# Kernel tuning notes

Hardware: AMD Instinct MI355X
Metric: run time of the kernel (lower is better)

Reference implementation:

```python
import jax, jax.numpy as jnp
import numpy as np

N = 8192
E = 262144
D_IN = 512
H1 = 32
H2 = 16
EPS = 1e-32


def setup_inputs() -> dict:
    key = jax.random.key(0)
    ks = jax.random.split(key, 7)
    X = jax.random.normal(ks[0], (N, D_IN), dtype=jnp.float32)
    edge_row = jax.random.randint(ks[1], (E,), 0, N, dtype=jnp.int64 if jax.config.read('jax_enable_x64') else jnp.int32).astype(jnp.int32)
    edge_col = jax.random.randint(ks[2], (E,), 0, N, dtype=jnp.int32)
    edge_val = jax.random.uniform(ks[3], (E,), dtype=jnp.float32)
    # glorot-style init scale (uniform in [-r, r])
    def glorot(k, din, dout):
        r = np.sqrt(6.0 / (din + dout)).astype(np.float32)
        return jax.random.uniform(k, (din, dout), dtype=jnp.float32, minval=-r, maxval=r)
    W0 = glorot(ks[4], D_IN, H1)
    W1 = glorot(ks[5], H1, H2)
    W2 = glorot(ks[6], H1, H2)
    return {"X": X, "edge_row": edge_row, "edge_col": edge_col,
            "edge_val": edge_val, "W0": W0, "W1": W1, "W2": W2}


def _spmm(edge_row, edge_col, edge_val, x):
    # out[i] = sum_j adj[i, j] * x[j] over COO edges
    gathered = edge_val[:, None] * x[edge_col]  # [E, d]
    return jax.ops.segment_sum(gathered, edge_row, num_segments=N)


def reference(X, edge_row, edge_col, edge_val, W0, W1, W2):
    # GraphConvSparse: adj @ (X @ W) then activation
    hidden = jax.nn.relu(_spmm(edge_row, edge_col, edge_val, X @ W0))      # [N, H1]
    mean = _spmm(edge_row, edge_col, edge_val, hidden @ W1)                 # [N, H2]
    std = _spmm(edge_row, edge_col, edge_val, hidden @ W2)                  # [N, H2]
    mean = jnp.maximum(mean, EPS)  # mean[mean < 1e-32] = 1e-32
    std = jnp.maximum(std, EPS)    # kept for parity; unused in eval path
    Z = mean  # eval mode: sampled_z = mean
    A_pred = jax.nn.sigmoid(Z @ Z.T)  # [N, N] dot-product decode
    return A_pred
```

## Files before the change

kernel.cpp:

```cpp
#include <hip/hip_runtime.h>

#define NN   8192
#define DIN  512
#define H1   32
#define H2   16
#define NE   262144
#define EPSV 1e-32f

__global__ __launch_bounds__(256) void k_xw0(const float* __restrict__ X,
                                             const float* __restrict__ W0,
                                             float* __restrict__ XW0) {
    int t = blockIdx.x * 256 + threadIdx.x;
    int r = t >> 5, c = t & 31;
    const float4* Xr = reinterpret_cast<const float4*>(X + (size_t)r * DIN);
    float acc = 0.f;
#pragma unroll 8
    for (int k4 = 0; k4 < DIN / 4; ++k4) {
        float4 x = Xr[k4];
        int k = k4 * 4;
        acc = fmaf(x.x, W0[(k + 0) * H1 + c], acc);
        acc = fmaf(x.y, W0[(k + 1) * H1 + c], acc);
        acc = fmaf(x.z, W0[(k + 2) * H1 + c], acc);
        acc = fmaf(x.w, W0[(k + 3) * H1 + c], acc);
    }
    XW0[t] = acc;
}

__global__ __launch_bounds__(256) void k_hist(const int* __restrict__ er,
                                              int* __restrict__ cnt) {
    int e = blockIdx.x * 256 + threadIdx.x;
    atomicAdd(&cnt[er[e]], 1);
}

__global__ __launch_bounds__(1024) void k_scan(const int* __restrict__ cnt,
                                               int* __restrict__ rptr,
                                               int* __restrict__ rfill) {
    __shared__ int part[1024];
    int tid = threadIdx.x;
    int local[8];
    int s = 0;
#pragma unroll
    for (int i = 0; i < 8; ++i) { local[i] = s; s += cnt[tid * 8 + i]; }
    part[tid] = s;
    __syncthreads();
    for (int off = 1; off < 1024; off <<= 1) {
        int v = (tid >= off) ? part[tid - off] : 0;
        __syncthreads();
        part[tid] += v;
        __syncthreads();
    }
    int base = (tid == 0) ? 0 : part[tid - 1];
#pragma unroll
    for (int i = 0; i < 8; ++i) {
        rptr[tid * 8 + i]  = base + local[i];
        rfill[tid * 8 + i] = base + local[i];
    }
    if (tid == 1023) rptr[8192] = part[1023];
}

__global__ __launch_bounds__(256) void k_scatter(const int* __restrict__ er,
                                                 const int* __restrict__ ec,
                                                 const float* __restrict__ ev,
                                                 int* __restrict__ rfill,
                                                 int* __restrict__ ccol,
                                                 float* __restrict__ cval) {
    int e = blockIdx.x * 256 + threadIdx.x;
    int p = atomicAdd(&rfill[er[e]], 1);
    ccol[p] = ec[e];
    cval[p] = ev[e];
}

__global__ __launch_bounds__(256) void k_spmm1(const int* __restrict__ rptr,
                                               const int* __restrict__ ccol,
                                               const float* __restrict__ cval,
                                               const float* __restrict__ XW0,
                                               float* __restrict__ hacc) {
    int t = blockIdx.x * 256 + threadIdx.x;
    int r = t >> 5, c = t & 31;
    int p = rptr[r], end = rptr[r + 1];
    float a0 = 0.f, a1 = 0.f;
    for (; p + 2 <= end; p += 2) {
        a0 = fmaf(cval[p],     XW0[ccol[p]     * H1 + c], a0);
        a1 = fmaf(cval[p + 1], XW0[ccol[p + 1] * H1 + c], a1);
    }
    if (p < end) a0 = fmaf(cval[p], XW0[ccol[p] * H1 + c], a0);
    hacc[t] = a0 + a1;
}

__global__ __launch_bounds__(256) void k_hw1(const float* __restrict__ hacc,
                                             const float* __restrict__ W1,
                                             float* __restrict__ HW1) {
    int t = blockIdx.x * 256 + threadIdx.x;
    int r = t >> 4, c = t & 15;
    const float* hr = hacc + r * H1;
    float acc = 0.f;
#pragma unroll
    for (int k = 0; k < H1; ++k)
        acc = fmaf(fmaxf(hr[k], 0.f), W1[k * H2 + c], acc);
    HW1[t] = acc;
}

__global__ __launch_bounds__(256) void k_spmm2(const int* __restrict__ rptr,
                                               const int* __restrict__ ccol,
                                               const float* __restrict__ cval,
                                               const float* __restrict__ HW1,
                                               float* __restrict__ mean) {
    int t = blockIdx.x * 256 + threadIdx.x;
    int r = t >> 4, c = t & 15;
    int p = rptr[r], end = rptr[r + 1];
    float a0 = 0.f, a1 = 0.f;
    for (; p + 2 <= end; p += 2) {
        a0 = fmaf(cval[p],     HW1[ccol[p]     * H2 + c], a0);
        a1 = fmaf(cval[p + 1], HW1[ccol[p + 1] * H2 + c], a1);
    }
    if (p < end) a0 = fmaf(cval[p], HW1[ccol[p] * H2 + c], a0);
    mean[t] = a0 + a1;
}

#define TI  128
#define PAD 20

__device__ __forceinline__ float sigm(float x) {
    return __fdividef(1.0f, 1.0f + __expf(-x));
}

__global__ __launch_bounds__(256) void k_decode(const float* __restrict__ Zm,
                                                float* __restrict__ out) {
    __shared__ float zi[TI * PAD];
    __shared__ float zj[TI * PAD];
    const int i0 = blockIdx.y * TI, j0 = blockIdx.x * TI;
    const int tid = threadIdx.x;

#pragma unroll
    for (int l = 0; l < 2; ++l) {
        int t = tid + l * 256;
        int r = t >> 2, c4 = (t & 3) * 4;
        float4 a = *reinterpret_cast<const float4*>(Zm + (size_t)(i0 + r) * H2 + c4);
        float4 b = *reinterpret_cast<const float4*>(Zm + (size_t)(j0 + r) * H2 + c4);
        a.x = fmaxf(a.x, EPSV); a.y = fmaxf(a.y, EPSV);
        a.z = fmaxf(a.z, EPSV); a.w = fmaxf(a.w, EPSV);
        b.x = fmaxf(b.x, EPSV); b.y = fmaxf(b.y, EPSV);
        b.z = fmaxf(b.z, EPSV); b.w = fmaxf(b.w, EPSV);
        *reinterpret_cast<float4*>(&zi[r * PAD + c4]) = a;
        *reinterpret_cast<float4*>(&zj[r * PAD + c4]) = b;
    }
    __syncthreads();

    const int tx = tid & 15, ty = tid >> 4;
    float acc[8][8] = {};
#pragma unroll
    for (int k4 = 0; k4 < 4; ++k4) {
        float4 ra[8], rb[8];
#pragma unroll
        for (int a = 0; a < 8; ++a)
            ra[a] = *reinterpret_cast<const float4*>(&zi[(ty * 8 + a) * PAD + k4 * 4]);
#pragma unroll
        for (int b = 0; b < 8; ++b)
            rb[b] = *reinterpret_cast<const float4*>(&zj[(tx * 8 + b) * PAD + k4 * 4]);
#pragma unroll
        for (int a = 0; a < 8; ++a)
#pragma unroll
            for (int b = 0; b < 8; ++b) {
                acc[a][b] = fmaf(ra[a].x, rb[b].x, acc[a][b]);
                acc[a][b] = fmaf(ra[a].y, rb[b].y, acc[a][b]);
                acc[a][b] = fmaf(ra[a].z, rb[b].z, acc[a][b]);
                acc[a][b] = fmaf(ra[a].w, rb[b].w, acc[a][b]);
            }
    }

#pragma unroll
    for (int a = 0; a < 8; ++a) {
        size_t rowbase = (size_t)(i0 + ty * 8 + a) * NN + j0 + tx * 8;
#pragma unroll
        for (int b4 = 0; b4 < 8; b4 += 4) {
            float4 o;
            o.x = sigm(acc[a][b4 + 0]);
            o.y = sigm(acc[a][b4 + 1]);
            o.z = sigm(acc[a][b4 + 2]);
            o.w = sigm(acc[a][b4 + 3]);
            *reinterpret_cast<float4*>(out + rowbase + b4) = o;
        }
    }
}

extern "C" void kernel_launch(void* const* d_in, const int* in_sizes, int n_in,
                              void* d_out, int out_size, void* d_ws, size_t ws_size,
                              hipStream_t stream) {
    const float* X  = (const float*)d_in[0];
    const int*   er = (const int*)d_in[1];
    const int*   ec = (const int*)d_in[2];
    const float* ev = (const float*)d_in[3];
    const float* W0 = (const float*)d_in[4];
    const float* W1 = (const float*)d_in[5];
    float* out = (float*)d_out;

    char* ws = (char*)d_ws;
    float* XW0  = (float*)(ws);
    float* hacc = (float*)(ws + (1 << 20));
    float* mean = (float*)(ws + (2 << 20));
    float* HW1  = (float*)(ws + (2 << 20) + (512 << 10));
    int*   cnt  = (int*)  (ws + (3 << 20));
    int*   rptr = (int*)  (ws + (3 << 20) + (64 << 10));
    int*   rfill= (int*)  (ws + (3 << 20) + (128 << 10));
    int*   ccol = (int*)  (ws + (3 << 20) + (192 << 10));
    float* cval = (float*)(ws + (4 << 20) + (192 << 10));

    hipMemsetAsync(cnt, 0, 32 << 10, stream);

    k_xw0    <<<NN * H1 / 256, 256, 0, stream>>>(X, W0, XW0);
    k_hist   <<<NE / 256, 256, 0, stream>>>(er, cnt);
    k_scan   <<<1, 1024, 0, stream>>>(cnt, rptr, rfill);
    k_scatter<<<NE / 256, 256, 0, stream>>>(er, ec, ev, rfill, ccol, cval);
    k_spmm1  <<<NN * H1 / 256, 256, 0, stream>>>(rptr, ccol, cval, XW0, hacc);
    k_hw1    <<<NN * H2 / 256, 256, 0, stream>>>(hacc, W1, HW1);
    k_spmm2  <<<NN * H2 / 256, 256, 0, stream>>>(rptr, ccol, cval, HW1, mean);
    k_decode <<<dim3(NN / TI, NN / TI), 256, 0, stream>>>(mean, out);
}
```

Measured before the change: 390.8 us.

## Split CSR row gathers across a block and swizzle decode shared-memory layout

Both sparse aggregation kernels now use one 256-thread block per row: edge groups work on different nonzeros in parallel, then a shared-memory reduction combines them. The aim is to expose more memory-level parallelism than one thread per output element walking the whole row sequentially. The decode kernel swaps the padded shared-memory layout for an XOR-swizzled one to cut LDS bank conflicts on the float4 reads. The costs are 8192 small blocks with mostly idle threads, since a row averages about 32 edges, plus a block barrier per row.

```diff
diff --git a/kernel.cpp b/kernel.cpp
--- a/kernel.cpp
+++ b/kernel.cpp
@@ -70,21 +70,26 @@
     cval[p] = ev[e];
 }
 
-__global__ __launch_bounds__(256) void k_spmm1(const int* __restrict__ rptr,
+__global__ __launch_bounds__(256) void k_gath1(const int* __restrict__ rptr,
                                                const int* __restrict__ ccol,
                                                const float* __restrict__ cval,
                                                const float* __restrict__ XW0,
                                                float* __restrict__ hacc) {
-    int t = blockIdx.x * 256 + threadIdx.x;
-    int r = t >> 5, c = t & 31;
-    int p = rptr[r], end = rptr[r + 1];
-    float a0 = 0.f, a1 = 0.f;
-    for (; p + 2 <= end; p += 2) {
-        a0 = fmaf(cval[p],     XW0[ccol[p]     * H1 + c], a0);
-        a1 = fmaf(cval[p + 1], XW0[ccol[p + 1] * H1 + c], a1);
-    }
-    if (p < end) a0 = fmaf(cval[p], XW0[ccol[p] * H1 + c], a0);
-    hacc[t] = a0 + a1;
+    __shared__ float sh[256];
+    int r = blockIdx.x;
+    int c = threadIdx.x & 31, g = threadIdx.x >> 5;
+    int start = rptr[r], end = rptr[r + 1];
+    float part = 0.f;
+    for (int p = start + g; p < end; p += 8)
+        part = fmaf(cval[p], XW0[ccol[p] * H1 + c], part);
+    sh[threadIdx.x] = part;
+    __syncthreads();
+    if (threadIdx.x < 32) {
+        float s = sh[c];
+#pragma unroll
+        for (int gg = 1; gg < 8; ++gg) s += sh[gg * 32 + c];
+        hacc[r * H1 + c] = s;
+    }
 }
 
 __global__ __launch_bounds__(256) void k_hw1(const float* __restrict__ hacc,
@@ -100,25 +105,29 @@
     HW1[t] = acc;
 }
 
-__global__ __launch_bounds__(256) void k_spmm2(const int* __restrict__ rptr,
+__global__ __launch_bounds__(256) void k_gath2(const int* __restrict__ rptr,
                                                const int* __restrict__ ccol,
                                                const float* __restrict__ cval,
                                                const float* __restrict__ HW1,
                                                float* __restrict__ mean) {
-    int t = blockIdx.x * 256 + threadIdx.x;
-    int r = t >> 4, c = t & 15;
-    int p = rptr[r], end = rptr[r + 1];
-    float a0 = 0.f, a1 = 0.f;
-    for (; p + 2 <= end; p += 2) {
-        a0 = fmaf(cval[p],     HW1[ccol[p]     * H2 + c], a0);
-        a1 = fmaf(cval[p + 1], HW1[ccol[p + 1] * H2 + c], a1);
-    }
-    if (p < end) a0 = fmaf(cval[p], HW1[ccol[p] * H2 + c], a0);
-    mean[t] = a0 + a1;
-}
-
-#define TI  128
-#define PAD 20
+    __shared__ float sh[256];
+    int r = blockIdx.x;
+    int c = threadIdx.x & 15, g = threadIdx.x >> 4;
+    int start = rptr[r], end = rptr[r + 1];
+    float part = 0.f;
+    for (int p = start + g; p < end; p += 16)
+        part = fmaf(cval[p], HW1[ccol[p] * H2 + c], part);
+    sh[threadIdx.x] = part;
+    __syncthreads();
+    if (threadIdx.x < 16) {
+        float s = sh[c];
+#pragma unroll
+        for (int gg = 1; gg < 16; ++gg) s += sh[gg * 16 + c];
+        mean[r * H2 + c] = s;
+    }
+}
+
+#define TI 128
 
 __device__ __forceinline__ float sigm(float x) {
     return __fdividef(1.0f, 1.0f + __expf(-x));
@@ -126,23 +135,26 @@
 
 __global__ __launch_bounds__(256) void k_decode(const float* __restrict__ Zm,
                                                 float* __restrict__ out) {
-    __shared__ float zi[TI * PAD];
-    __shared__ float zj[TI * PAD];
+    __shared__ float zi[TI * 16];
+    __shared__ float zj[TI * 32];
     const int i0 = blockIdx.y * TI, j0 = blockIdx.x * TI;
     const int tid = threadIdx.x;
 
 #pragma unroll
     for (int l = 0; l < 2; ++l) {
         int t = tid + l * 256;
-        int r = t >> 2, c4 = (t & 3) * 4;
-        float4 a = *reinterpret_cast<const float4*>(Zm + (size_t)(i0 + r) * H2 + c4);
-        float4 b = *reinterpret_cast<const float4*>(Zm + (size_t)(j0 + r) * H2 + c4);
+        int r = t >> 2, q = t & 3;
+        float4 a = *reinterpret_cast<const float4*>(Zm + (size_t)(i0 + r) * H2 + q * 4);
+        float4 b = *reinterpret_cast<const float4*>(Zm + (size_t)(j0 + r) * H2 + q * 4);
         a.x = fmaxf(a.x, EPSV); a.y = fmaxf(a.y, EPSV);
         a.z = fmaxf(a.z, EPSV); a.w = fmaxf(a.w, EPSV);
         b.x = fmaxf(b.x, EPSV); b.y = fmaxf(b.y, EPSV);
         b.z = fmaxf(b.z, EPSV); b.w = fmaxf(b.w, EPSV);
-        *reinterpret_cast<float4*>(&zi[r * PAD + c4]) = a;
-        *reinterpret_cast<float4*>(&zj[r * PAD + c4]) = b;
+        int g  = (r >> 3);
+        int qs = q ^ (g & 3);
+        int p  = (q ^ (g & 3)) | (g & 4);
+        *reinterpret_cast<float4*>(&zi[r * 16 + qs * 4]) = a;
+        *reinterpret_cast<float4*>(&zj[r * 32 + p  * 4]) = b;
     }
     __syncthreads();
 
@@ -151,12 +163,14 @@
 #pragma unroll
     for (int k4 = 0; k4 < 4; ++k4) {
         float4 ra[8], rb[8];
+        const int qi = (k4 ^ (ty & 3)) * 4;
+        const int pj = ((k4 ^ (tx & 3)) | (tx & 4)) * 4;
 #pragma unroll
         for (int a = 0; a < 8; ++a)
-            ra[a] = *reinterpret_cast<const float4*>(&zi[(ty * 8 + a) * PAD + k4 * 4]);
+            ra[a] = *reinterpret_cast<const float4*>(&zi[(ty * 8 + a) * 16 + qi]);
 #pragma unroll
         for (int b = 0; b < 8; ++b)
-            rb[b] = *reinterpret_cast<const float4*>(&zj[(tx * 8 + b) * PAD + k4 * 4]);
+            rb[b] = *reinterpret_cast<const float4*>(&zj[(tx * 8 + b) * 32 + pj]);
 #pragma unroll
         for (int a = 0; a < 8; ++a)
 #pragma unroll
@@ -211,8 +225,8 @@
     k_hist   <<<NE / 256, 256, 0, stream>>>(er, cnt);
     k_scan   <<<1, 1024, 0, stream>>>(cnt, rptr, rfill);
     k_scatter<<<NE / 256, 256, 0, stream>>>(er, ec, ev, rfill, ccol, cval);
-    k_spmm1  <<<NN * H1 / 256, 256, 0, stream>>>(rptr, ccol, cval, XW0, hacc);
+    k_gath1  <<<NN, 256, 0, stream>>>(rptr, ccol, cval, XW0, hacc);
     k_hw1    <<<NN * H2 / 256, 256, 0, stream>>>(hacc, W1, HW1);
-    k_spmm2  <<<NN * H2 / 256, 256, 0, stream>>>(rptr, ccol, cval, HW1, mean);
+    k_gath2  <<<NN, 256, 0, stream>>>(rptr, ccol, cval, HW1, mean);
     k_decode <<<dim3(NN / TI, NN / TI), 256, 0, stream>>>(mean, out);
 }
```

Measured after the change: 383.8 us. No clear change (-1.8%).
